# Kernel tuning notes

Measured on AMD Instinct MI355X. Metric: run time of the kernel, lower is better.

The kernel has to match this reference:

```python
import jax, jax.numpy as jnp
import numpy as np

N, M, D = 62, 512, 256  # parts, batch samples (P*K = 64*8), hidden dim
K_PER_ID = 8
MARGIN = 0.2


def setup_inputs() -> dict:
    key = jax.random.key(0)
    k1, = jax.random.split(key, 1)
    feature = jax.random.normal(k1, (N, M, D), dtype=jnp.float32)
    # P*K structured labels (uniform class sizes are REQUIRED by the original
    # masked_select(...).view(n, m, -1) reshape): 64 ids, 8 samples each,
    # identical label layout for every part row n.
    row = jnp.arange(M, dtype=jnp.int64) // K_PER_ID  # [M]
    label = jnp.tile(row[None, :], (N, 1))            # [N, M]
    return {"feature": feature, "label": label}


def _safe_sqrt(x):
    # sqrt(relu(x)) with a zero (finite) gradient at x <= 0, matching the
    # forward values of torch.sqrt(F.relu(x)) exactly.
    pos = x > 0
    return jnp.where(pos, jnp.sqrt(jnp.where(pos, x, 1.0)), 0.0)


def reference(feature, label):
    # feature: [n, m, d], label: [n, m]
    sq = jnp.sum(feature * feature, axis=2)                       # [n, m]
    gram = jnp.einsum('nmd,nkd->nmk', feature, feature)           # [n, m, m]
    d2 = sq[:, :, None] + sq[:, None, :] - 2.0 * gram             # [n, m, m]
    dist = _safe_sqrt(jnp.maximum(d2, 0.0))                       # [n, m, m]

    dist_mean = jnp.mean(dist, axis=(1, 2))                       # [n]

    pos_mask = label[:, :, None] == label[:, None, :]             # [n, m, m]
    # hard positive: max dist over same-label columns (incl. self)
    hard_hp = jnp.max(jnp.where(pos_mask, dist, -jnp.inf), axis=2)   # [n, m]
    # hard negative: min dist over different-label columns
    hard_hn = jnp.min(jnp.where(pos_mask, jnp.inf, dist), axis=2)    # [n, m]

    hard_loss = jax.nn.relu(MARGIN + hard_hp - hard_hn)           # [n, m]
    hard_loss_mean = jnp.mean(hard_loss, axis=1)                  # [n]
    return hard_loss_mean, dist_mean
```

## Files before the change

### kernel.cpp

```cpp
#include <hip/hip_runtime.h>

#define N_PARTS 62
#define M_SAMP  512
#define D_DIM   256
#define MARGIN  0.2f
#define ROWS    (N_PARTS * M_SAMP)
#define PART_ELEMS (M_SAMP * D_DIM)

typedef unsigned short ushort_t;
typedef __attribute__((ext_vector_type(8))) short bf16x8;
typedef __attribute__((ext_vector_type(4))) float f32x4;

__device__ __forceinline__ ushort_t bf16_rne(float f) {
    unsigned u = __float_as_uint(f);
    unsigned r = u + 0x7fffu + ((u >> 16) & 1u);
    return (ushort_t)(r >> 16);
}

__device__ __forceinline__ void async_copy16(const ushort_t* g, ushort_t* l) {
    __builtin_amdgcn_global_load_lds(
        (const __attribute__((address_space(1))) unsigned int*)g,
        (__attribute__((address_space(3))) unsigned int*)l,
        16, 0, 0);
}

__global__ __launch_bounds__(256) void prep_kernel(const float* __restrict__ feat,
                                                   ushort_t* __restrict__ Fb,
                                                   float* __restrict__ sq,
                                                   float* __restrict__ out) {
    const int gid  = blockIdx.x * 256 + threadIdx.x;
    const int lane = threadIdx.x & 63;
    const int row  = gid >> 6;
    const int part = row >> 9, rp = row & 511;
    const float4 v = ((const float4*)(feat + (size_t)row * D_DIM))[lane];
    ushort4 us;
    us.x = bf16_rne(v.x); us.y = bf16_rne(v.y);
    us.z = bf16_rne(v.z); us.w = bf16_rne(v.w);
    const float fx = __uint_as_float((unsigned)us.x << 16);
    const float fy = __uint_as_float((unsigned)us.y << 16);
    const float fz = __uint_as_float((unsigned)us.z << 16);
    const float fw = __uint_as_float((unsigned)us.w << 16);
    const int c = lane >> 3;
    const int q = (lane >> 1) & 3;
    const int j = (lane & 1) * 4;
    const int s = q ^ ((rp >> 1) & 3);
    *(ushort4*)(Fb + (size_t)part * PART_ELEMS + ((c * M_SAMP + rp) * 32) + s * 8 + j) = us;
    float ssum = fx * fx + fy * fy + fz * fz + fw * fw;
    #pragma unroll
    for (int off = 32; off > 0; off >>= 1) ssum += __shfl_xor(ssum, off);
    if (lane == 0) sq[row] = ssum;
    if (gid < 2 * N_PARTS) out[gid] = 0.0f;
}

__global__ __launch_bounds__(256) void fused_triplet_kernel(const ushort_t* __restrict__ Fb,
                                                            const float* __restrict__ sq,
                                                            float* __restrict__ out) {
    const int n  = blockIdx.x;
    const int r0 = blockIdx.y * 64;
    const int tid = threadIdx.x;
    const int wave = tid >> 6, lane = tid & 63;
    const int wy = wave >> 1, wx = wave & 1;
    const ushort_t* F = Fb + (size_t)n * PART_ELEMS;
    const float* SQ = sq + n * M_SAMP;

    __shared__ ushort_t a0[64 * 32],  a1[64 * 32];
    __shared__ ushort_t b0[128 * 32], b1[128 * 32];
    __shared__ float mrg[2][64][3];

    f32x4 acc[2][4] = {};
    float hp_r[2][4], hn_r[2][4], ds_r[2][4];
    #pragma unroll
    for (int mi = 0; mi < 2; ++mi)
        #pragma unroll
        for (int p = 0; p < 4; ++p) { hp_r[mi][p] = 0.f; hn_r[mi][p] = 1e30f; ds_r[mi][p] = 0.f; }

    float sqr[2][4];
    #pragma unroll
    for (int mi = 0; mi < 2; ++mi)
        #pragma unroll
        for (int p = 0; p < 4; ++p)
            sqr[mi][p] = SQ[r0 + wy * 32 + mi * 16 + (lane >> 4) * 4 + p];

    auto stage = [&](int c, ushort_t* la, ushort_t* lb) {
        const int kchunk = c & 7;
        const int cb = (c >> 3) * 128;
        const ushort_t* Ab = F + ((size_t)kchunk * M_SAMP + r0) * 32;
        const ushort_t* Bb = F + ((size_t)kchunk * M_SAMP + cb) * 32;
        async_copy16(Ab + (wave * 16) * 32 + lane * 8, la + (wave * 16) * 32);
        #pragma unroll
        for (int j = 0; j < 2; ++j)
            async_copy16(Bb + (wave * 32 + j * 16) * 32 + lane * 8,
                         lb + (wave * 32 + j * 16) * 32);
    };

    auto compute = [&](const ushort_t* la, const ushort_t* lb) {
        bf16x8 af[2], bf[4];
        #pragma unroll
        for (int mi = 0; mi < 2; ++mi) {
            const int ra = wy * 32 + mi * 16 + (lane & 15);
            const int sa = (lane >> 4) ^ ((ra >> 1) & 3);
            af[mi] = *(const bf16x8*)((const char*)la + ra * 64 + sa * 16);
        }
        #pragma unroll
        for (int ni = 0; ni < 4; ++ni) {
            const int rb = wx * 64 + ni * 16 + (lane & 15);
            const int sb = (lane >> 4) ^ ((rb >> 1) & 3);
            bf[ni] = *(const bf16x8*)((const char*)lb + rb * 64 + sb * 16);
        }
        #pragma unroll
        for (int mi = 0; mi < 2; ++mi)
            #pragma unroll
            for (int ni = 0; ni < 4; ++ni)
                acc[mi][ni] = __builtin_amdgcn_mfma_f32_16x16x32_bf16(
                    af[mi], bf[ni], acc[mi][ni], 0, 0, 0);
    };

    auto fold = [&](int ct) {
        float sqc[4];
        #pragma unroll
        for (int ni = 0; ni < 4; ++ni)
            sqc[ni] = SQ[ct * 128 + wx * 64 + ni * 16 + (lane & 15)];
        #pragma unroll
        for (int mi = 0; mi < 2; ++mi) {
            #pragma unroll
            for (int p = 0; p < 4; ++p) {
                const int Rg = (r0 + wy * 32 + mi * 16 + (lane >> 4) * 4 + p) >> 3;
                const float sr = sqr[mi][p];
                float ds = ds_r[mi][p], hp = hp_r[mi][p], hn = hn_r[mi][p];
                #pragma unroll
                for (int ni = 0; ni < 4; ++ni) {
                    const int C = ct * 128 + wx * 64 + ni * 16 + (lane & 15);
                    const float d2 = sr + sqc[ni] - 2.f * acc[mi][ni][p];
                    const float d  = sqrtf(fmaxf(d2, 0.f));
                    ds += d;
                    if (Rg == (C >> 3)) hp = fmaxf(hp, d);
                    else                hn = fminf(hn, d);
                }
                ds_r[mi][p] = ds; hp_r[mi][p] = hp; hn_r[mi][p] = hn;
            }
        }
        #pragma unroll
        for (int mi = 0; mi < 2; ++mi)
            #pragma unroll
            for (int ni = 0; ni < 4; ++ni)
                acc[mi][ni] = (f32x4){0.f, 0.f, 0.f, 0.f};
    };

    stage(0, a0, b0);
    for (int cc = 0; cc < 32; cc += 2) {
        __syncthreads();
        stage(cc + 1, a1, b1);
        compute(a0, b0);
        __syncthreads();
        if (cc + 2 < 32) stage(cc + 2, a0, b0);
        compute(a1, b1);
        if (((cc + 1) & 7) == 7) fold((cc + 1) >> 3);
    }

    #pragma unroll
    for (int off = 1; off < 16; off <<= 1) {
        #pragma unroll
        for (int mi = 0; mi < 2; ++mi)
            #pragma unroll
            for (int p = 0; p < 4; ++p) {
                ds_r[mi][p] += __shfl_xor(ds_r[mi][p], off);
                hp_r[mi][p]  = fmaxf(hp_r[mi][p], __shfl_xor(hp_r[mi][p], off));
                hn_r[mi][p]  = fminf(hn_r[mi][p], __shfl_xor(hn_r[mi][p], off));
            }
    }
    if ((lane & 15) == 0) {
        const int q = lane >> 4;
        #pragma unroll
        for (int mi = 0; mi < 2; ++mi)
            #pragma unroll
            for (int p = 0; p < 4; ++p) {
                const int rl = wy * 32 + mi * 16 + q * 4 + p;
                mrg[wx][rl][0] = hp_r[mi][p];
                mrg[wx][rl][1] = hn_r[mi][p];
                mrg[wx][rl][2] = ds_r[mi][p];
            }
    }
    __syncthreads();
    if (tid < 64) {
        const float hp = fmaxf(mrg[0][tid][0], mrg[1][tid][0]);
        const float hn = fminf(mrg[0][tid][1], mrg[1][tid][1]);
        float bd = mrg[0][tid][2] + mrg[1][tid][2];
        float bl = fmaxf(MARGIN + hp - hn, 0.f);
        #pragma unroll
        for (int off = 32; off > 0; off >>= 1) {
            bl += __shfl_xor(bl, off);
            bd += __shfl_xor(bd, off);
        }
        if (lane == 0) {
            atomicAdd(&out[n],           bl * (1.0f / 512.0f));
            atomicAdd(&out[N_PARTS + n], bd * (1.0f / (512.0f * 512.0f)));
        }
    }
}

extern "C" void kernel_launch(void* const* d_in, const int* in_sizes, int n_in,
                              void* d_out, int out_size, void* d_ws, size_t ws_size,
                              hipStream_t stream) {
    const float* feat = (const float*)d_in[0];
    float* out = (float*)d_out;

    ushort_t* Fb = (ushort_t*)d_ws;
    float* sq    = (float*)((char*)d_ws + (size_t)ROWS * D_DIM * 2);

    prep_kernel<<<dim3(ROWS / 4), 256, 0, stream>>>(feat, Fb, sq, out);
    fused_triplet_kernel<<<dim3(N_PARTS, 8), 256, 0, stream>>>(Fb, sq, out);
}
```

Measured before the change: 104.8 us.

## Widen block to cover all 512 columns per 64-row tile with 8 waves

The fused triplet kernel now uses 512 threads (8 waves), and each wave owns 64 of the 512 columns for a 64-row tile. The full B panel per k-chunk is staged in LDS, so the K loop runs once over 8 chunks instead of 32 iterations with column-tile folds. This removes the repeated per-column-tile fold passes and the extra A reloads. In exchange it uses more LDS (about 72KB of double-buffered B) and a 4x4 accumulator per wave, which may lower occupancy and adds an 8-way cross-wave merge.

```diff
diff --git a/kernel.cpp b/kernel.cpp
--- a/kernel.cpp
+++ b/kernel.cpp
@@ -52,139 +52,109 @@
     if (gid < 2 * N_PARTS) out[gid] = 0.0f;
 }
 
-__global__ __launch_bounds__(256) void fused_triplet_kernel(const ushort_t* __restrict__ Fb,
-                                                            const float* __restrict__ sq,
-                                                            float* __restrict__ out) {
+__global__ __launch_bounds__(512, 4) void fused_triplet_kernel(const ushort_t* __restrict__ Fb,
+                                                               const float* __restrict__ sq,
+                                                               float* __restrict__ out) {
     const int n  = blockIdx.x;
     const int r0 = blockIdx.y * 64;
     const int tid = threadIdx.x;
     const int wave = tid >> 6, lane = tid & 63;
-    const int wy = wave >> 1, wx = wave & 1;
     const ushort_t* F = Fb + (size_t)n * PART_ELEMS;
     const float* SQ = sq + n * M_SAMP;
 
     __shared__ ushort_t a0[64 * 32],  a1[64 * 32];
-    __shared__ ushort_t b0[128 * 32], b1[128 * 32];
-    __shared__ float mrg[2][64][3];
+    __shared__ ushort_t b0[512 * 32], b1[512 * 32];
+    __shared__ float mrg[8][64][3];
 
-    f32x4 acc[2][4] = {};
-    float hp_r[2][4], hn_r[2][4], ds_r[2][4];
-    #pragma unroll
-    for (int mi = 0; mi < 2; ++mi)
+    f32x4 acc[4][4] = {};
+
+    auto stage = [&](int kchunk, ushort_t* la, ushort_t* lb) {
+        const ushort_t* base = F + (size_t)kchunk * (M_SAMP * 32);
         #pragma unroll
-        for (int p = 0; p < 4; ++p) { hp_r[mi][p] = 0.f; hn_r[mi][p] = 1e30f; ds_r[mi][p] = 0.f; }
-
-    float sqr[2][4];
-    #pragma unroll
-    for (int mi = 0; mi < 2; ++mi)
-        #pragma unroll
-        for (int p = 0; p < 4; ++p)
-            sqr[mi][p] = SQ[r0 + wy * 32 + mi * 16 + (lane >> 4) * 4 + p];
-
-    auto stage = [&](int c, ushort_t* la, ushort_t* lb) {
-        const int kchunk = c & 7;
-        const int cb = (c >> 3) * 128;
-        const ushort_t* Ab = F + ((size_t)kchunk * M_SAMP + r0) * 32;
-        const ushort_t* Bb = F + ((size_t)kchunk * M_SAMP + cb) * 32;
-        async_copy16(Ab + (wave * 16) * 32 + lane * 8, la + (wave * 16) * 32);
-        #pragma unroll
-        for (int j = 0; j < 2; ++j)
-            async_copy16(Bb + (wave * 32 + j * 16) * 32 + lane * 8,
-                         lb + (wave * 32 + j * 16) * 32);
+        for (int i = 0; i < 4; ++i) {
+            const int rb = wave * 64 + i * 16;
+            async_copy16(base + rb * 32 + lane * 8, lb + rb * 32);
+        }
+        if (wave < 4)
+            async_copy16(base + (r0 + wave * 16) * 32 + lane * 8, la + (wave * 16) * 32);
     };
 
     auto compute = [&](const ushort_t* la, const ushort_t* lb) {
-        bf16x8 af[2], bf[4];
+        bf16x8 af[4], bf[4];
         #pragma unroll
-        for (int mi = 0; mi < 2; ++mi) {
-            const int ra = wy * 32 + mi * 16 + (lane & 15);
+        for (int mi = 0; mi < 4; ++mi) {
+            const int ra = mi * 16 + (lane & 15);
             const int sa = (lane >> 4) ^ ((ra >> 1) & 3);
-            af[mi] = *(const bf16x8*)((const char*)la + ra * 64 + sa * 16);
+            af[mi] = *(const bf16x8*)(la + ra * 32 + sa * 8);
         }
         #pragma unroll
         for (int ni = 0; ni < 4; ++ni) {
-            const int rb = wx * 64 + ni * 16 + (lane & 15);
+            const int rb = wave * 64 + ni * 16 + (lane & 15);
             const int sb = (lane >> 4) ^ ((rb >> 1) & 3);
-            bf[ni] = *(const bf16x8*)((const char*)lb + rb * 64 + sb * 16);
+            bf[ni] = *(const bf16x8*)(lb + rb * 32 + sb * 8);
         }
         #pragma unroll
-        for (int mi = 0; mi < 2; ++mi)
+        for (int mi = 0; mi < 4; ++mi)
             #pragma unroll
             for (int ni = 0; ni < 4; ++ni)
                 acc[mi][ni] = __builtin_amdgcn_mfma_f32_16x16x32_bf16(
                     af[mi], bf[ni], acc[mi][ni], 0, 0, 0);
     };
 
-    auto fold = [&](int ct) {
-        float sqc[4];
-        #pragma unroll
-        for (int ni = 0; ni < 4; ++ni)
-            sqc[ni] = SQ[ct * 128 + wx * 64 + ni * 16 + (lane & 15)];
-        #pragma unroll
-        for (int mi = 0; mi < 2; ++mi) {
-            #pragma unroll
-            for (int p = 0; p < 4; ++p) {
-                const int Rg = (r0 + wy * 32 + mi * 16 + (lane >> 4) * 4 + p) >> 3;
-                const float sr = sqr[mi][p];
-                float ds = ds_r[mi][p], hp = hp_r[mi][p], hn = hn_r[mi][p];
-                #pragma unroll
-                for (int ni = 0; ni < 4; ++ni) {
-                    const int C = ct * 128 + wx * 64 + ni * 16 + (lane & 15);
-                    const float d2 = sr + sqc[ni] - 2.f * acc[mi][ni][p];
-                    const float d  = sqrtf(fmaxf(d2, 0.f));
-                    ds += d;
-                    if (Rg == (C >> 3)) hp = fmaxf(hp, d);
-                    else                hn = fminf(hn, d);
-                }
-                ds_r[mi][p] = ds; hp_r[mi][p] = hp; hn_r[mi][p] = hn;
-            }
-        }
-        #pragma unroll
-        for (int mi = 0; mi < 2; ++mi)
-            #pragma unroll
-            for (int ni = 0; ni < 4; ++ni)
-                acc[mi][ni] = (f32x4){0.f, 0.f, 0.f, 0.f};
-    };
-
     stage(0, a0, b0);
-    for (int cc = 0; cc < 32; cc += 2) {
+    #pragma unroll
+    for (int cc = 0; cc < 8; cc += 2) {
         __syncthreads();
         stage(cc + 1, a1, b1);
         compute(a0, b0);
         __syncthreads();
-        if (cc + 2 < 32) stage(cc + 2, a0, b0);
+        if (cc + 2 < 8) stage(cc + 2, a0, b0);
         compute(a1, b1);
-        if (((cc + 1) & 7) == 7) fold((cc + 1) >> 3);
     }
 
+    float sqc[4];
     #pragma unroll
-    for (int off = 1; off < 16; off <<= 1) {
+    for (int ni = 0; ni < 4; ++ni)
+        sqc[ni] = SQ[wave * 64 + ni * 16 + (lane & 15)];
+    #pragma unroll
+    for (int mi = 0; mi < 4; ++mi) {
         #pragma unroll
-        for (int mi = 0; mi < 2; ++mi)
+        for (int p = 0; p < 4; ++p) {
+            const int rl = mi * 16 + (lane >> 4) * 4 + p;
+            const int R  = r0 + rl;
+            const float sr = SQ[R];
+            float ds = 0.f, hp = 0.f, hn = 1e30f;
             #pragma unroll
-            for (int p = 0; p < 4; ++p) {
-                ds_r[mi][p] += __shfl_xor(ds_r[mi][p], off);
-                hp_r[mi][p]  = fmaxf(hp_r[mi][p], __shfl_xor(hp_r[mi][p], off));
-                hn_r[mi][p]  = fminf(hn_r[mi][p], __shfl_xor(hn_r[mi][p], off));
+            for (int ni = 0; ni < 4; ++ni) {
+                const int C = wave * 64 + ni * 16 + (lane & 15);
+                const float d2 = sr + sqc[ni] - 2.f * acc[mi][ni][p];
+                const float d  = sqrtf(fmaxf(d2, 0.f));
+                ds += d;
+                if ((R >> 3) == (C >> 3)) hp = fmaxf(hp, d);
+                else                      hn = fminf(hn, d);
             }
-    }
-    if ((lane & 15) == 0) {
-        const int q = lane >> 4;
-        #pragma unroll
-        for (int mi = 0; mi < 2; ++mi)
             #pragma unroll
-            for (int p = 0; p < 4; ++p) {
-                const int rl = wy * 32 + mi * 16 + q * 4 + p;
-                mrg[wx][rl][0] = hp_r[mi][p];
-                mrg[wx][rl][1] = hn_r[mi][p];
-                mrg[wx][rl][2] = ds_r[mi][p];
+            for (int off = 1; off < 16; off <<= 1) {
+                ds += __shfl_xor(ds, off);
+                hp = fmaxf(hp, __shfl_xor(hp, off));
+                hn = fminf(hn, __shfl_xor(hn, off));
             }
+            if ((lane & 15) == 0) {
+                mrg[wave][rl][0] = hp;
+                mrg[wave][rl][1] = hn;
+                mrg[wave][rl][2] = ds;
+            }
+        }
     }
     __syncthreads();
     if (tid < 64) {
-        const float hp = fmaxf(mrg[0][tid][0], mrg[1][tid][0]);
-        const float hn = fminf(mrg[0][tid][1], mrg[1][tid][1]);
-        float bd = mrg[0][tid][2] + mrg[1][tid][2];
+        float hp = 0.f, hn = 1e30f, bd = 0.f;
+        #pragma unroll
+        for (int w = 0; w < 8; ++w) {
+            hp = fmaxf(hp, mrg[w][tid][0]);
+            hn = fminf(hn, mrg[w][tid][1]);
+            bd += mrg[w][tid][2];
+        }
         float bl = fmaxf(MARGIN + hp - hn, 0.f);
         #pragma unroll
         for (int off = 32; off > 0; off >>= 1) {
@@ -208,5 +178,5 @@
     float* sq    = (float*)((char*)d_ws + (size_t)ROWS * D_DIM * 2);
 
     prep_kernel<<<dim3(ROWS / 4), 256, 0, stream>>>(feat, Fb, sq, out);
-    fused_triplet_kernel<<<dim3(N_PARTS, 8), 256, 0, stream>>>(Fb, sq, out);
+    fused_triplet_kernel<<<dim3(N_PARTS, 8), 512, 0, stream>>>(Fb, sq, out);
 }
```

Measured after the change: 106.3 us. Within noise of the previous version (+1.4%).
